# Optimization experiments

Hardware: AMD Instinct MI355X
Metric: run time of the kernel (lower is better)

Reference implementation:

```python
import jax, jax.numpy as jnp
import numpy as np


def _layer_norm(x, g, b, eps=1e-12):
    mu = jnp.mean(x, axis=-1, keepdims=True)
    var = jnp.mean(jnp.square(x - mu), axis=-1, keepdims=True)
    return (x - mu) * jax.lax.rsqrt(var + eps) * g + b


def setup_inputs() -> dict:
    B, S, H = 16, 512, 1024
    key = jax.random.key(0)
    ks = jax.random.split(key, 8)
    p = lambda k, sh: 0.02 * jax.random.normal(k, sh, jnp.float32)
    return {
        "sequence_output": jax.random.normal(ks[0], (B, S, H), jnp.float32),
        "p_mask": jax.random.randint(ks[1], (B, S), 0, 2).astype(jnp.float32),
        "w_start": p(ks[2], (H, 1)),
        "b_start": jnp.zeros((1,), jnp.float32),
        "w_end0": p(ks[3], (2 * H, H)),
        "b_end0": jnp.zeros((H,), jnp.float32),
        "ln_g": jnp.ones((H,), jnp.float32),
        "ln_b": jnp.zeros((H,), jnp.float32),
        "w_end1": p(ks[4], (H, 1)),
        "b_end1": jnp.zeros((1,), jnp.float32),
        "w_ans0": p(ks[5], (2 * H, H)),
        "b_ans0": jnp.zeros((H,), jnp.float32),
        "w_ans1": p(ks[6], (H, 1)),
        "start_n_top": 5,
        "end_n_top": 5,
    }


def reference(sequence_output, p_mask, w_start, b_start, w_end0, b_end0,
              ln_g, ln_b, w_end1, b_end1, w_ans0, b_ans0, w_ans1,
              start_n_top, end_n_top):
    # Inference (beam-search) branch of ALBertQALayer. Layout kept as [B,S,H]
    # (original transposes to [S,B,H]; math is identical).
    B, S, H = sequence_output.shape
    NEG = jnp.float32(1e30)

    # ---- start logits ----
    start_logits = (sequence_output @ w_start).squeeze(-1) + b_start          # [B,S]
    start_masked = start_logits * (1.0 - p_mask) - NEG * p_mask
    start_log_probs = jax.nn.log_softmax(start_masked, axis=-1)
    start_top_log_probs, start_top_index = jax.lax.top_k(start_log_probs, start_n_top)  # [B,K1]

    # ---- end logits conditioned on top-k starts ----
    start_features = jnp.take_along_axis(
        sequence_output, start_top_index[:, :, None], axis=1)                 # [B,K1,H]
    end_input = jnp.concatenate([
        jnp.broadcast_to(sequence_output[:, :, None, :], (B, S, start_n_top, H)),
        jnp.broadcast_to(start_features[:, None, :, :], (B, S, start_n_top, H)),
    ], axis=-1)                                                               # [B,S,K1,2H]
    end_h = jnp.tanh(jnp.einsum('bskd,dh->bskh', end_input, w_end0) + b_end0)
    end_h = _layer_norm(end_h, ln_g, ln_b)
    end_logits = jnp.einsum('bskh,ho->bsko', end_h, w_end1).squeeze(-1) + b_end1  # [B,S,K1]
    end_logits = jnp.transpose(end_logits, (0, 2, 1))                         # [B,K1,S]
    end_masked = end_logits * (1.0 - p_mask[:, None, :]) - NEG * p_mask[:, None, :]
    end_log_probs = jax.nn.log_softmax(end_masked, axis=-1)
    end_top_log_probs, end_top_index = jax.lax.top_k(end_log_probs, end_n_top)  # [B,K1,K2]
    end_top_log_probs = end_top_log_probs.reshape(B, start_n_top * end_n_top)
    end_top_index = end_top_index.reshape(B, start_n_top * end_n_top)

    # ---- answer-class (is-impossible) logits ----
    cls_feature = sequence_output[:, 0, :]                                    # one_hot(0) gather
    start_p = jax.nn.softmax(start_masked, axis=-1)
    start_feature = jnp.einsum('bs,bsh->bh', start_p, sequence_output)
    ans = jnp.tanh(jnp.concatenate([start_feature, cls_feature], axis=-1) @ w_ans0 + b_ans0)
    cls_logits = (ans @ w_ans1).squeeze(-1)                                   # [B]

    return (start_top_log_probs, start_top_index,
            end_top_log_probs, end_top_index, cls_logits)
```

## Files before the change

kernel.cpp:

```cpp
#include <hip/hip_runtime.h>
#include <math.h>

#define BB 16
#define SS 512
#define HH 1024
#define KT 5
#define NEGV 1e30f

typedef __attribute__((ext_vector_type(8))) short short8_t;
typedef __attribute__((ext_vector_type(4))) float f32x4;

__device__ __forceinline__ float wave_sum(float v) {
    for (int off = 32; off; off >>= 1) v += __shfl_down(v, off);
    return v;
}

__device__ __forceinline__ unsigned short bf16rn(float x) {
    unsigned u = __float_as_uint(x);
    return (unsigned short)((u + 0x7fffu + ((u >> 16) & 1u)) >> 16);
}

__device__ __forceinline__ void split2(float x, unsigned short& h, unsigned short& l) {
    h = bf16rn(x);
    float hf = __uint_as_float(((unsigned)h) << 16);
    l = bf16rn(x - hf);
}

__device__ __forceinline__ float tanh_fast(float x) {
    float e = __expf(2.0f * x);
    return 1.0f - 2.0f * __builtin_amdgcn_rcpf(e + 1.0f);
}

__device__ __forceinline__ void gld16(const short* g, char* l) {
    __builtin_amdgcn_global_load_lds((const __attribute__((address_space(1))) void*)g,
                                     (__attribute__((address_space(3))) void*)l, 16, 0, 0);
}

template <bool WRITE_P>
__device__ void softmax_topk_vals(float x0, float x1, float* __restrict__ p_out,
                                  float* __restrict__ val_out, float* __restrict__ idxf_out,
                                  int* __restrict__ idxi_out) {
    const int t = threadIdx.x;
    __shared__ float scr[4];
    __shared__ float sv[4];
    __shared__ int si[4];
    __shared__ int wi_s;

    float m = fmaxf(x0, x1);
    for (int off = 32; off; off >>= 1) m = fmaxf(m, __shfl_down(m, off));
    if ((t & 63) == 0) scr[t >> 6] = m;
    __syncthreads();
    m = fmaxf(fmaxf(scr[0], scr[1]), fmaxf(scr[2], scr[3]));
    __syncthreads();

    float e0 = expf(x0 - m), e1 = expf(x1 - m);
    float ssum = wave_sum(e0 + e1);
    if ((t & 63) == 0) scr[t >> 6] = ssum;
    __syncthreads();
    ssum = scr[0] + scr[1] + scr[2] + scr[3];
    __syncthreads();

    if (WRITE_P) {
        p_out[t] = e0 / ssum;
        p_out[t + 256] = e1 / ssum;
    }
    const float lse = m + logf(ssum);

    float v0 = x0, v1 = x1;
    for (int k = 0; k < KT; ++k) {
        float bv;
        int bi;
        if (v0 >= v1) { bv = v0; bi = t; } else { bv = v1; bi = t + 256; }
        for (int off = 32; off; off >>= 1) {
            float ov = __shfl_down(bv, off);
            int oi = __shfl_down(bi, off);
            if (ov > bv || (ov == bv && oi < bi)) { bv = ov; bi = oi; }
        }
        if ((t & 63) == 0) { sv[t >> 6] = bv; si[t >> 6] = bi; }
        __syncthreads();
        if (t == 0) {
            float fv = sv[0];
            int fi = si[0];
            for (int w = 1; w < 4; ++w)
                if (sv[w] > fv || (sv[w] == fv && si[w] < fi)) { fv = sv[w]; fi = si[w]; }
            wi_s = fi;
            val_out[k] = fv - lse;
            idxf_out[k] = (float)fi;
            if (idxi_out) idxi_out[k] = fi;
        }
        __syncthreads();
        const int wi = wi_s;
        if (wi == t) v0 = -INFINITY;
        else if (wi == t + 256) v1 = -INFINITY;
        __syncthreads();
    }
}

__global__ void k_mega(const float* __restrict__ seq, const float* __restrict__ w_end0,
                       const float* __restrict__ pm, const float* __restrict__ w_start,
                       const float* __restrict__ b_start, const float* __restrict__ ln_g,
                       const float* __restrict__ ln_b, const float* __restrict__ w_end1,
                       short* __restrict__ wpk_hi, short* __restrict__ wpk_lo,
                       short* __restrict__ apk_hi, short* __restrict__ apk_lo,
                       float* __restrict__ sm, float* __restrict__ scal) {
    const int bid = blockIdx.x;
    const int t = threadIdx.x;
    __shared__ float scr8[8];

    if (bid < 4096) {
        const size_t g = (size_t)bid * 256 + t;
        const int l = g & 63;
        const int mtl = (g >> 6) & 7;
        const int ks = (g >> 9) & 31;
        const int bm = g >> 14;
        const int row = bm * 128 + mtl * 16 + (l & 15);
        const int k0 = ks * 32 + (l >> 4) * 8;
        const float4 v0 = *(const float4*)(seq + (size_t)row * HH + k0);
        const float4 v1 = *(const float4*)(seq + (size_t)row * HH + k0 + 4);
        float xs[8] = {v0.x, v0.y, v0.z, v0.w, v1.x, v1.y, v1.z, v1.w};
        unsigned short h[8], lo[8];
#pragma unroll
        for (int j = 0; j < 8; ++j) split2(xs[j], h[j], lo[j]);
        short8_t hv, lv;
#pragma unroll
        for (int j = 0; j < 8; ++j) { hv[j] = (short)h[j]; lv[j] = (short)lo[j]; }
        *(short8_t*)(apk_hi + g * 8) = hv;
        *(short8_t*)(apk_lo + g * 8) = lv;
    } else if (bid < 4608) {
        const int bid2 = bid - 4096;
        const int nt = bid2 & 63;
        const int yy = bid2 >> 6;
        const int n_idx = t & 15;
        const int g = (t >> 4) & 3;
        const int kq = t >> 6;
        const int kblk = yy * 4 + kq;
        const int k0 = kblk * 32 + g * 8;
        unsigned short hs[8], ls[8];
#pragma unroll
        for (int j = 0; j < 8; ++j) {
            float v = w_end0[(size_t)(k0 + j) * HH + nt * 16 + n_idx];
            split2(v, hs[j], ls[j]);
        }
        const size_t fi = (((size_t)nt * 32 + kblk) * 64 + (g * 16 + n_idx)) * 8;
        short8_t hv, lv;
#pragma unroll
        for (int j = 0; j < 8; ++j) { hv[j] = (short)hs[j]; lv[j] = (short)ls[j]; }
        *(short8_t*)(wpk_hi + fi) = hv;
        *(short8_t*)(wpk_lo + fi) = lv;
    } else if (bid < 6656) {
        const int l = t & 63;
        const int row = (bid - 4608) * 4 + (t >> 6);
        const float4* rp = (const float4*)(seq + (size_t)row * HH);
        const float4* wp = (const float4*)w_start;
        float d = 0.f;
#pragma unroll
        for (int q = 0; q < 4; ++q) {
            float4 a = rp[q * 64 + l];
            float4 w = wp[q * 64 + l];
            d += a.x * w.x + a.y * w.y + a.z * w.z + a.w * w.w;
        }
        d = wave_sum(d);
        if (l == 0) {
            float m = pm[row];
            sm[row] = (d + b_start[0]) * (1.f - m) - NEGV * m;
        }
    } else {
        float4 g = ((const float4*)ln_g)[t];
        float4 w = ((const float4*)w_end1)[t];
        float4 b = ((const float4*)ln_b)[t];
        float gw = g.x * w.x + g.y * w.y + g.z * w.z + g.w * w.w;
        float bw = b.x * w.x + b.y * w.y + b.z * w.z + b.w * w.w;
        gw = wave_sum(gw);
        bw = wave_sum(bw);
        if ((t & 63) == 0) { scr8[t >> 6] = gw; scr8[4 + (t >> 6)] = bw; }
        __syncthreads();
        if (t == 0) {
            scal[0] = scr8[0] + scr8[1] + scr8[2] + scr8[3];
            scal[1] = scr8[4] + scr8[5] + scr8[6] + scr8[7];
        }
    }
}

__global__ void k_softmax_start(const float* __restrict__ sm, float* __restrict__ sp,
                                float* __restrict__ dout, int* __restrict__ idx) {
    const int b = blockIdx.x;
    const int t = threadIdx.x;
    const float* x = sm + (size_t)b * SS;
    softmax_topk_vals<true>(x[t], x[t + 256], sp + (size_t)b * SS,
                            dout + b * KT, dout + 80 + b * KT, idx + b * KT);
}

__global__ void k_mid(const float* __restrict__ seq, const int* __restrict__ idx,
                      const float* __restrict__ w_end0, float* __restrict__ Cpart,
                      const float* __restrict__ sp, float* __restrict__ partial) {
    __shared__ float shA[80 * 132];
    __shared__ float shW[16 * 132];
    __shared__ int growL[80];
    const int bid = blockIdx.x;
    const int t = threadIdx.x;

    if (bid < 512) {
        const int c = bid & 63;
        const int kc = bid >> 6;
        if (t < 80) growL[t] = (t / KT) * SS + idx[t];
        __syncthreads();
        for (int i = 0; i < 40; ++i) {
            const int e = i * 256 + t;
            const int r = e >> 7, d = e & 127;
            shA[r * 132 + d] = seq[(size_t)growL[r] * HH + kc * 128 + d];
        }
#pragma unroll
        for (int p = 0; p < 8; ++p) {
            const int e = p * 256 + t;
            const int d = e >> 4, j = e & 15;
            shW[j * 132 + d] = w_end0[(size_t)(HH + kc * 128 + d) * HH + c * 16 + j];
        }
        __syncthreads();
        const int j = t & 15, rg = t >> 4;
        const float4* A4 = (const float4*)shA;
        const float4* W4 = (const float4*)shW;
        float acc[5] = {0.f, 0.f, 0.f, 0.f, 0.f};
        for (int d4 = 0; d4 < 32; ++d4) {
            float4 wv = W4[j * 33 + d4];
#pragma unroll
            for (int i = 0; i < 5; ++i) {
                float4 av = A4[(rg + 16 * i) * 33 + d4];
                acc[i] += av.x * wv.x + av.y * wv.y + av.z * wv.z + av.w * wv.w;
            }
        }
#pragma unroll
        for (int i = 0; i < 5; ++i)
            Cpart[((size_t)kc * 80 + rg + 16 * i) * HH + c * 16 + j] = acc[i];
    } else {
        const int bid2 = bid - 512;
        const int chunk = bid2 & 31;
        const int b = bid2 >> 5;
        if (t < 16) shA[t] = sp[b * SS + chunk * 16 + t];
        __syncthreads();
        float4 acc = make_float4(0.f, 0.f, 0.f, 0.f);
        const float4* base = (const float4*)(seq + ((size_t)b * SS + chunk * 16) * HH);
        for (int s = 0; s < 16; ++s) {
            float4 v = base[(size_t)s * 256 + t];
            float ps = shA[s];
            acc.x = fmaf(ps, v.x, acc.x);
            acc.y = fmaf(ps, v.y, acc.y);
            acc.z = fmaf(ps, v.z, acc.z);
            acc.w = fmaf(ps, v.w, acc.w);
        }
        ((float4*)partial)[(size_t)(b * 32 + chunk) * 256 + t] = acc;
    }
}

__global__ void k_red(const float* __restrict__ Cpart, const float* __restrict__ b_end0,
                      float* __restrict__ Cb, const float* __restrict__ seq,
                      const float* __restrict__ partial, float* __restrict__ feat) {
    const int bid = blockIdx.x;
    const int t = threadIdx.x;
    if (bid < 80) {
        const int bk = bid;
#pragma unroll
        for (int q = 0; q < 4; ++q) {
            const int h = q * 256 + t;
            float s = b_end0[h];
#pragma unroll
            for (int kc = 0; kc < 8; ++kc) s += Cpart[((size_t)kc * 80 + bk) * HH + h];
            Cb[(size_t)bk * HH + h] = s;
        }
    } else {
        const int b = bid - 80;
        for (int q = 0; q < 4; ++q) {
            const int h = q * 256 + t;
            float s = 0.f;
            for (int c = 0; c < 32; ++c) s += partial[(size_t)(b * 32 + c) * HH + h];
            feat[(size_t)b * 2048 + h] = s;
            feat[(size_t)b * 2048 + HH + h] = seq[(size_t)b * SS * HH + h];
        }
    }
}

__global__ void k_ans(const float* __restrict__ feat, const float* __restrict__ w_ans0,
                      float* __restrict__ anspart) {
    __shared__ float A[16 * 132];
    __shared__ float W[16 * 132];
    const int c = blockIdx.x & 63;
    const int kc = blockIdx.x >> 6;
    const int t = threadIdx.x;
#pragma unroll
    for (int i = 0; i < 8; ++i) {
        const int e = i * 256 + t;
        const int b = e >> 7, d = e & 127;
        A[b * 132 + d] = feat[(size_t)b * 2048 + kc * 128 + d];
    }
#pragma unroll
    for (int p = 0; p < 8; ++p) {
        const int e = p * 256 + t;
        const int d = e >> 4, j = e & 15;
        W[j * 132 + d] = w_ans0[(size_t)(kc * 128 + d) * HH + c * 16 + j];
    }
    __syncthreads();
    const int j = t & 15, b = t >> 4;
    const float4* A4 = (const float4*)A;
    const float4* W4 = (const float4*)W;
    float acc = 0.f;
    for (int d4 = 0; d4 < 32; ++d4) {
        float4 wv = W4[j * 33 + d4];
        float4 av = A4[b * 33 + d4];
        acc += av.x * wv.x + av.y * wv.y + av.z * wv.z + av.w * wv.w;
    }
    anspart[((size_t)kc * 16 + b) * HH + c * 16 + j] = acc;
}

__global__ __launch_bounds__(256, 2)
void k_gemm(const short* __restrict__ apk_hi, const short* __restrict__ apk_lo,
            const short* __restrict__ wpk_hi, const short* __restrict__ wpk_lo,
            const float* __restrict__ Cb, const float* __restrict__ ln_g,
            const float* __restrict__ w_end1, float* __restrict__ part) {
    extern __shared__ char smem[];
    const int t = threadIdx.x;
    const int l = t & 63, w = t >> 6;
    const int wr = w >> 1, wc = w & 1;
    const int wg = blockIdx.x;
    const int xcd = wg & 7;
    const int local = wg >> 3;
    const int bm = xcd * 8 + (local >> 3);
    const int bn = local & 7;
    const int row0 = bm * 128;
    const int b = row0 >> 9;

    f32x4 acc[4][4];
#pragma unroll
    for (int m = 0; m < 4; ++m)
#pragma unroll
        for (int n = 0; n < 4; ++n) acc[m][n] = (f32x4){0.f, 0.f, 0.f, 0.f};

#define STAGE(buf, ks)                                                                   \
    {                                                                                    \
        const size_t abase = (size_t)(bm * 32 + (ks)) * 8 * 512;                         \
        const size_t wbase = ((size_t)(bn * 8) * 32 + (ks)) * 512;                       \
        char* lb = smem + (buf) * 32768;                                                 \
        _Pragma("unroll") for (int q = 0; q < 2; ++q) {                                  \
            const int fr = w + q * 4;                                                    \
            gld16(apk_hi + abase + fr * 512 + l * 8, lb + fr * 1024);                    \
            gld16(apk_lo + abase + fr * 512 + l * 8, lb + 8192 + fr * 1024);             \
            gld16(wpk_hi + wbase + (size_t)fr * 32 * 512 + l * 8, lb + 16384 + fr * 1024); \
            gld16(wpk_lo + wbase + (size_t)fr * 32 * 512 + l * 8, lb + 24576 + fr * 1024); \
        }                                                                                \
    }

    STAGE(0, 0);
    __syncthreads();

    for (int ks = 0; ks < 32; ++ks) {
        const int buf = ks & 1;
        if (ks < 31) STAGE(buf ^ 1, ks + 1);
        {
            const char* base_ = smem + buf * 32768;
            short8_t ah[4], al[4], wh[4], wl[4];
#pragma unroll
            for (int m = 0; m < 4; ++m) {
                const int mtl = wr * 4 + m;
                ah[m] = *(const short8_t*)(base_ + (mtl << 10) + (l << 4));
                al[m] = *(const short8_t*)(base_ + 8192 + (mtl << 10) + (l << 4));
            }
#pragma unroll
            for (int n = 0; n < 4; ++n) {
                const int ntl = wc * 4 + n;
                wh[n] = *(const short8_t*)(base_ + 16384 + (ntl << 10) + (l << 4));
                wl[n] = *(const short8_t*)(base_ + 24576 + (ntl << 10) + (l << 4));
            }
#pragma unroll
            for (int n = 0; n < 4; ++n)
#pragma unroll
                for (int m = 0; m < 4; ++m) {
                    acc[m][n] = __builtin_amdgcn_mfma_f32_16x16x32_bf16(ah[m], wh[n], acc[m][n], 0, 0, 0);
                    acc[m][n] = __builtin_amdgcn_mfma_f32_16x16x32_bf16(al[m], wh[n], acc[m][n], 0, 0, 0);
                    acc[m][n] = __builtin_amdgcn_mfma_f32_16x16x32_bf16(ah[m], wl[n], acc[m][n], 0, 0, 0);
                }
        }
        __syncthreads();
    }
#undef STAGE

    float cbv[KT][4], gwv[4];
#pragma unroll
    for (int n = 0; n < 4; ++n) {
        const int col = bn * 128 + wc * 64 + n * 16 + (l & 15);
        gwv[n] = ln_g[col] * w_end1[col];
#pragma unroll
        for (int k = 0; k < KT; ++k) cbv[k][n] = Cb[(size_t)(b * KT + k) * HH + col];
    }
    float* scr = (float*)smem;

    for (int k = 0; k < KT; ++k) {
        float S[4][4], Q[4][4], G[4][4];
#pragma unroll
        for (int m = 0; m < 4; ++m)
#pragma unroll
            for (int r = 0; r < 4; ++r) { S[m][r] = 0.f; Q[m][r] = 0.f; G[m][r] = 0.f; }
#pragma unroll
        for (int n = 0; n < 4; ++n) {
            const float cb = cbv[k][n];
            const float gwn = gwv[n];
#pragma unroll
            for (int m = 0; m < 4; ++m)
#pragma unroll
                for (int r = 0; r < 4; ++r) {
                    float v = tanh_fast(acc[m][n][r] + cb);
                    S[m][r] += v;
                    Q[m][r] += v * v;
                    G[m][r] += v * gwn;
                }
        }
        for (int msk = 1; msk < 16; msk <<= 1) {
#pragma unroll
            for (int m = 0; m < 4; ++m)
#pragma unroll
                for (int r = 0; r < 4; ++r) {
                    S[m][r] += __shfl_xor(S[m][r], msk);
                    Q[m][r] += __shfl_xor(Q[m][r], msk);
                    G[m][r] += __shfl_xor(G[m][r], msk);
                }
        }
        if ((l & 15) == 0) {
            const int gg = l >> 4;
#pragma unroll
            for (int m = 0; m < 4; ++m)
#pragma unroll
                for (int r = 0; r < 4; ++r) {
                    const int row = wr * 64 + m * 16 + gg * 4 + r;
                    float* sp_ = scr + ((wc * 128 + row) * KT + k) * 3;
                    sp_[0] = S[m][r];
                    sp_[1] = Q[m][r];
                    sp_[2] = G[m][r];
                }
        }
    }
    __syncthreads();

#pragma unroll
    for (int i = 0; i < 3; ++i) {
        const int idx = i * 256 + t;
        if (idx < 128 * KT) {
            const int row = idx / KT, k = idx % KT;
            const float* a_ = scr + ((0 * 128 + row) * KT + k) * 3;
            const float* b_ = scr + ((1 * 128 + row) * KT + k) * 3;
            float4 o;
            o.x = a_[0] + b_[0];
            o.y = a_[1] + b_[1];
            o.z = a_[2] + b_[2];
            o.w = 0.f;
            *(float4*)(part + (((size_t)bn * (BB * SS) + row0 + row) * KT + k) * 4) = o;
        }
    }
}

__global__ void k_final(const float* __restrict__ part, const float* __restrict__ p_mask,
                        const float* __restrict__ scal, const float* __restrict__ b_end1,
                        const float* __restrict__ anspart, const float* __restrict__ b_ans0,
                        const float* __restrict__ w_ans1, float* __restrict__ out) {
    const int bid = blockIdx.x;
    const int t = threadIdx.x;
    __shared__ float rscr[4];

    if (bid < 80) {
        const int b = bid / KT, k = bid % KT;
        const float GW1 = scal[0], BW1 = scal[1], be1 = b_end1[0];
        float x01[2];
#pragma unroll
        for (int h = 0; h < 2; ++h) {
            const int s = h * 256 + t;
            const int row = b * SS + s;
            float S = 0.f, Q = 0.f, G = 0.f;
#pragma unroll
            for (int bn = 0; bn < 8; ++bn) {
                float4 v = *(const float4*)(part + (((size_t)bn * (BB * SS) + row) * KT + k) * 4);
                S += v.x;
                Q += v.y;
                G += v.z;
            }
            const float mu = S * (1.f / HH);
            const float var = Q * (1.f / HH) - mu * mu;
            const float rs = rsqrtf(var + 1e-12f);
            const float logit = rs * (G - mu * GW1) + BW1 + be1;
            const float pm = p_mask[row];
            x01[h] = logit * (1.f - pm) - NEGV * pm;
        }
        softmax_topk_vals<false>(x01[0], x01[1], nullptr,
                                 out + 160 + b * 25 + k * KT, out + 560 + b * 25 + k * KT, nullptr);
    } else {
        const int b = bid - 80;
        float dsum = 0.f;
#pragma unroll
        for (int q = 0; q < 4; ++q) {
            const int h = q * 256 + t;
            float s = b_ans0[h];
#pragma unroll
            for (int kc = 0; kc < 16; ++kc) s += anspart[((size_t)kc * 16 + b) * HH + h];
            dsum += tanhf(s) * w_ans1[h];
        }
        dsum = wave_sum(dsum);
        if ((t & 63) == 0) rscr[t >> 6] = dsum;
        __syncthreads();
        if (t == 0) out[960 + b] = rscr[0] + rscr[1] + rscr[2] + rscr[3];
    }
}

extern "C" void kernel_launch(void* const* d_in, const int* in_sizes, int n_in,
                              void* d_out, int out_size, void* d_ws, size_t ws_size,
                              hipStream_t stream) {
    const float* seq     = (const float*)d_in[0];
    const float* p_mask  = (const float*)d_in[1];
    const float* w_start = (const float*)d_in[2];
    const float* b_start = (const float*)d_in[3];
    const float* w_end0  = (const float*)d_in[4];
    const float* b_end0  = (const float*)d_in[5];
    const float* ln_g    = (const float*)d_in[6];
    const float* ln_b    = (const float*)d_in[7];
    const float* w_end1  = (const float*)d_in[8];
    const float* b_end1  = (const float*)d_in[9];
    const float* w_ans0  = (const float*)d_in[10];
    const float* b_ans0  = (const float*)d_in[11];
    const float* w_ans1  = (const float*)d_in[12];
    float* out = (float*)d_out;

    float* sm      = (float*)d_ws;
    float* sp      = sm + BB * SS;
    float* partial = sp + BB * SS;
    float* feat    = partial + BB * 32 * HH;
    float* Cb      = feat + BB * 2048;
    float* Cpart   = Cb + 80 * HH;
    float* anspart = Cpart + 8 * 80 * HH;
    float* scal    = anspart + 16 * BB * HH;
    int*   idx     = (int*)(scal + 16);
    float* part    = (float*)(((uintptr_t)(idx + 80) + 255) & ~(uintptr_t)255);
    short* wpk_hi  = (short*)(part + 8 * BB * SS * KT * 4);
    short* wpk_lo  = wpk_hi + (1 << 20);
    short* apk_hi  = wpk_lo + (1 << 20);
    short* apk_lo  = apk_hi + (1 << 23);

    hipLaunchKernelGGL(k_mega, dim3(6657), dim3(256), 0, stream,
                       seq, w_end0, p_mask, w_start, b_start, ln_g, ln_b, w_end1,
                       wpk_hi, wpk_lo, apk_hi, apk_lo, sm, scal);
    hipLaunchKernelGGL(k_softmax_start, dim3(BB), dim3(256), 0, stream, sm, sp, out, idx);
    hipLaunchKernelGGL(k_mid, dim3(1024), dim3(256), 0, stream,
                       seq, idx, w_end0, Cpart, sp, partial);
    hipLaunchKernelGGL(k_red, dim3(96), dim3(256), 0, stream,
                       Cpart, b_end0, Cb, seq, partial, feat);
    hipLaunchKernelGGL(k_ans, dim3(1024), dim3(256), 0, stream, feat, w_ans0, anspart);
    hipLaunchKernelGGL(k_gemm, dim3(512), dim3(256), 65536, stream,
                       apk_hi, apk_lo, wpk_hi, wpk_lo, Cb, ln_g, w_end1, part);
    hipLaunchKernelGGL(k_final, dim3(96), dim3(256), 0, stream,
                       part, p_mask, scal, b_end1, anspart, b_ans0, w_ans1, out);
}
```

Before: 129.7 us.

## Load GEMM weight fragments directly to registers, halve LDS, raise occupancy

In k_gemm the split-bf16 weight tiles (hi/lo) are now loaded straight from global memory into registers, with the hi part prefetched one k-step ahead, instead of being staged through LDS. Only the activation tiles stay double-buffered in shared memory, which halves dynamic LDS from 64KB to 32KB, and launch bounds are raised to 3 blocks per CU. The MFMA section is also wrapped in s_setprio. The aim is to cut LDS traffic and footprint so more blocks fit per CU, at the cost of more register pressure and direct global loads that each wave issues separately for its own weight columns.

```diff
diff --git a/kernel.cpp b/kernel.cpp
--- a/kernel.cpp
+++ b/kernel.cpp
@@ -310,7 +310,7 @@
     anspart[((size_t)kc * 16 + b) * HH + c * 16 + j] = acc;
 }
 
-__global__ __launch_bounds__(256, 2)
+__global__ __launch_bounds__(256, 3)
 void k_gemm(const short* __restrict__ apk_hi, const short* __restrict__ apk_lo,
             const short* __restrict__ wpk_hi, const short* __restrict__ wpk_lo,
             const float* __restrict__ Cb, const float* __restrict__ ln_g,
@@ -333,49 +333,61 @@
 #pragma unroll
         for (int n = 0; n < 4; ++n) acc[m][n] = (f32x4){0.f, 0.f, 0.f, 0.f};
 
-#define STAGE(buf, ks)                                                                   \
-    {                                                                                    \
-        const size_t abase = (size_t)(bm * 32 + (ks)) * 8 * 512;                         \
-        const size_t wbase = ((size_t)(bn * 8) * 32 + (ks)) * 512;                       \
-        char* lb = smem + (buf) * 32768;                                                 \
-        _Pragma("unroll") for (int q = 0; q < 2; ++q) {                                  \
-            const int fr = w + q * 4;                                                    \
-            gld16(apk_hi + abase + fr * 512 + l * 8, lb + fr * 1024);                    \
-            gld16(apk_lo + abase + fr * 512 + l * 8, lb + 8192 + fr * 1024);             \
-            gld16(wpk_hi + wbase + (size_t)fr * 32 * 512 + l * 8, lb + 16384 + fr * 1024); \
-            gld16(wpk_lo + wbase + (size_t)fr * 32 * 512 + l * 8, lb + 24576 + fr * 1024); \
-        }                                                                                \
-    }
+    const short8_t* WH = (const short8_t*)wpk_hi;
+    const short8_t* WL = (const short8_t*)wpk_lo;
+    const size_t wb = ((size_t)(bn * 8 + wc * 4)) * 2048 + l;
+
+#define STAGE(buf, ks)                                                     \
+    {                                                                      \
+        const size_t abase = (size_t)(bm * 32 + (ks)) * 4096;              \
+        char* lb = smem + (buf) * 16384;                                   \
+        gld16(apk_hi + abase + (2 * w) * 512 + l * 8, lb + (2 * w) * 1024);        \
+        gld16(apk_hi + abase + (2 * w + 1) * 512 + l * 8, lb + (2 * w + 1) * 1024); \
+        gld16(apk_lo + abase + (2 * w) * 512 + l * 8, lb + 8192 + (2 * w) * 1024);  \
+        gld16(apk_lo + abase + (2 * w + 1) * 512 + l * 8, lb + 8192 + (2 * w + 1) * 1024); \
+    }
+
+    short8_t wCh[4], wNh[4], wl_[4];
 
     STAGE(0, 0);
+#pragma unroll
+    for (int n = 0; n < 4; ++n) wCh[n] = WH[wb + n * 2048];
     __syncthreads();
 
     for (int ks = 0; ks < 32; ++ks) {
         const int buf = ks & 1;
-        if (ks < 31) STAGE(buf ^ 1, ks + 1);
-        {
-            const char* base_ = smem + buf * 32768;
-            short8_t ah[4], al[4], wh[4], wl[4];
+        if (ks < 31) {
+            STAGE(buf ^ 1, ks + 1);
+#pragma unroll
+            for (int n = 0; n < 4; ++n) wNh[n] = WH[wb + n * 2048 + (ks + 1) * 64];
+        }
+#pragma unroll
+        for (int n = 0; n < 4; ++n) wl_[n] = WL[wb + n * 2048 + ks * 64];
+        const char* base_ = smem + buf * 16384;
+        short8_t ah[4], al[4];
+#pragma unroll
+        for (int m = 0; m < 4; ++m) {
+            const int mtl = wr * 4 + m;
+            ah[m] = *(const short8_t*)(base_ + (mtl << 10) + (l << 4));
+            al[m] = *(const short8_t*)(base_ + 8192 + (mtl << 10) + (l << 4));
+        }
+        __builtin_amdgcn_s_setprio(1);
+#pragma unroll
+        for (int n = 0; n < 4; ++n)
 #pragma unroll
             for (int m = 0; m < 4; ++m) {
-                const int mtl = wr * 4 + m;
-                ah[m] = *(const short8_t*)(base_ + (mtl << 10) + (l << 4));
-                al[m] = *(const short8_t*)(base_ + 8192 + (mtl << 10) + (l << 4));
+                acc[m][n] = __builtin_amdgcn_mfma_f32_16x16x32_bf16(ah[m], wCh[n], acc[m][n], 0, 0, 0);
+                acc[m][n] = __builtin_amdgcn_mfma_f32_16x16x32_bf16(al[m], wCh[n], acc[m][n], 0, 0, 0);
             }
 #pragma unroll
-            for (int n = 0; n < 4; ++n) {
-                const int ntl = wc * 4 + n;
-                wh[n] = *(const short8_t*)(base_ + 16384 + (ntl << 10) + (l << 4));
-                wl[n] = *(const short8_t*)(base_ + 24576 + (ntl << 10) + (l << 4));
-            }
-#pragma unroll
-            for (int n = 0; n < 4; ++n)
-#pragma unroll
-                for (int m = 0; m < 4; ++m) {
-                    acc[m][n] = __builtin_amdgcn_mfma_f32_16x16x32_bf16(ah[m], wh[n], acc[m][n], 0, 0, 0);
-                    acc[m][n] = __builtin_amdgcn_mfma_f32_16x16x32_bf16(al[m], wh[n], acc[m][n], 0, 0, 0);
-                    acc[m][n] = __builtin_amdgcn_mfma_f32_16x16x32_bf16(ah[m], wl[n], acc[m][n], 0, 0, 0);
-                }
+        for (int n = 0; n < 4; ++n)
+#pragma unroll
+            for (int m = 0; m < 4; ++m)
+                acc[m][n] = __builtin_amdgcn_mfma_f32_16x16x32_bf16(ah[m], wl_[n], acc[m][n], 0, 0, 0);
+        __builtin_amdgcn_s_setprio(0);
+        if (ks < 31) {
+#pragma unroll
+            for (int n = 0; n < 4; ++n) wCh[n] = wNh[n];
         }
         __syncthreads();
     }
@@ -547,7 +559,7 @@
     hipLaunchKernelGGL(k_red, dim3(96), dim3(256), 0, stream,
                        Cpart, b_end0, Cb, seq, partial, feat);
     hipLaunchKernelGGL(k_ans, dim3(1024), dim3(256), 0, stream, feat, w_ans0, anspart);
-    hipLaunchKernelGGL(k_gemm, dim3(512), dim3(256), 65536, stream,
+    hipLaunchKernelGGL(k_gemm, dim3(512), dim3(256), 32768, stream,
                        apk_hi, apk_lo, wpk_hi, wpk_lo, Cb, ln_g, w_end1, part);
     hipLaunchKernelGGL(k_final, dim3(96), dim3(256), 0, stream,
                        part, p_mask, scal, b_end1, anspart, b_ans0, w_ans1, out);
```

Result: no change. 131.3 us (+1.2%).

## Fuse activation bf16 hi/lo split into GEMM, loading fp32 seq directly to LDS

Applied to the files above, without the earlier changes.

Drops the pre-pass in the mega kernel that split the 32 MB fp32 sequence into packed bf16 hi/lo buffers. The GEMM now streams fp32 rows straight into LDS with an XOR swizzle and does the split in registers before the MFMAs. This removes a full write and re-read of the packed activations, at the cost of extra ALU work and LDS reads inside the GEMM inner loop. It also raises wave priority around the MFMA block.

```diff
diff --git a/kernel.cpp b/kernel.cpp
--- a/kernel.cpp
+++ b/kernel.cpp
@@ -31,7 +31,7 @@
     return 1.0f - 2.0f * __builtin_amdgcn_rcpf(e + 1.0f);
 }
 
-__device__ __forceinline__ void gld16(const short* g, char* l) {
+__device__ __forceinline__ void gld16(const void* g, char* l) {
     __builtin_amdgcn_global_load_lds((const __attribute__((address_space(1))) void*)g,
                                      (__attribute__((address_space(3))) void*)l, 16, 0, 0);
 }
@@ -101,35 +101,14 @@
                        const float* __restrict__ b_start, const float* __restrict__ ln_g,
                        const float* __restrict__ ln_b, const float* __restrict__ w_end1,
                        short* __restrict__ wpk_hi, short* __restrict__ wpk_lo,
-                       short* __restrict__ apk_hi, short* __restrict__ apk_lo,
                        float* __restrict__ sm, float* __restrict__ scal) {
     const int bid = blockIdx.x;
     const int t = threadIdx.x;
     __shared__ float scr8[8];
 
-    if (bid < 4096) {
-        const size_t g = (size_t)bid * 256 + t;
-        const int l = g & 63;
-        const int mtl = (g >> 6) & 7;
-        const int ks = (g >> 9) & 31;
-        const int bm = g >> 14;
-        const int row = bm * 128 + mtl * 16 + (l & 15);
-        const int k0 = ks * 32 + (l >> 4) * 8;
-        const float4 v0 = *(const float4*)(seq + (size_t)row * HH + k0);
-        const float4 v1 = *(const float4*)(seq + (size_t)row * HH + k0 + 4);
-        float xs[8] = {v0.x, v0.y, v0.z, v0.w, v1.x, v1.y, v1.z, v1.w};
-        unsigned short h[8], lo[8];
-#pragma unroll
-        for (int j = 0; j < 8; ++j) split2(xs[j], h[j], lo[j]);
-        short8_t hv, lv;
-#pragma unroll
-        for (int j = 0; j < 8; ++j) { hv[j] = (short)h[j]; lv[j] = (short)lo[j]; }
-        *(short8_t*)(apk_hi + g * 8) = hv;
-        *(short8_t*)(apk_lo + g * 8) = lv;
-    } else if (bid < 4608) {
-        const int bid2 = bid - 4096;
-        const int nt = bid2 & 63;
-        const int yy = bid2 >> 6;
+    if (bid < 512) {
+        const int nt = bid & 63;
+        const int yy = bid >> 6;
         const int n_idx = t & 15;
         const int g = (t >> 4) & 3;
         const int kq = t >> 6;
@@ -147,9 +126,9 @@
         for (int j = 0; j < 8; ++j) { hv[j] = (short)hs[j]; lv[j] = (short)ls[j]; }
         *(short8_t*)(wpk_hi + fi) = hv;
         *(short8_t*)(wpk_lo + fi) = lv;
-    } else if (bid < 6656) {
+    } else if (bid < 2560) {
         const int l = t & 63;
-        const int row = (bid - 4608) * 4 + (t >> 6);
+        const int row = (bid - 512) * 4 + (t >> 6);
         const float4* rp = (const float4*)(seq + (size_t)row * HH);
         const float4* wp = (const float4*)w_start;
         float d = 0.f;
@@ -311,10 +290,10 @@
 }
 
 __global__ __launch_bounds__(256, 2)
-void k_gemm(const short* __restrict__ apk_hi, const short* __restrict__ apk_lo,
-            const short* __restrict__ wpk_hi, const short* __restrict__ wpk_lo,
-            const float* __restrict__ Cb, const float* __restrict__ ln_g,
-            const float* __restrict__ w_end1, float* __restrict__ part) {
+void k_gemm(const float* __restrict__ seq, const short* __restrict__ wpk_hi,
+            const short* __restrict__ wpk_lo, const float* __restrict__ Cb,
+            const float* __restrict__ ln_g, const float* __restrict__ w_end1,
+            float* __restrict__ part) {
     extern __shared__ char smem[];
     const int t = threadIdx.x;
     const int l = t & 63, w = t >> 6;
@@ -333,22 +312,42 @@
 #pragma unroll
         for (int n = 0; n < 4; ++n) acc[m][n] = (f32x4){0.f, 0.f, 0.f, 0.f};
 
-#define STAGE(buf, ks)                                                                   \
-    {                                                                                    \
-        const size_t abase = (size_t)(bm * 32 + (ks)) * 8 * 512;                         \
-        const size_t wbase = ((size_t)(bn * 8) * 32 + (ks)) * 512;                       \
-        char* lb = smem + (buf) * 32768;                                                 \
-        _Pragma("unroll") for (int q = 0; q < 2; ++q) {                                  \
-            const int fr = w + q * 4;                                                    \
-            gld16(apk_hi + abase + fr * 512 + l * 8, lb + fr * 1024);                    \
-            gld16(apk_lo + abase + fr * 512 + l * 8, lb + 8192 + fr * 1024);             \
-            gld16(wpk_hi + wbase + (size_t)fr * 32 * 512 + l * 8, lb + 16384 + fr * 1024); \
-            gld16(wpk_lo + wbase + (size_t)fr * 32 * 512 + l * 8, lb + 24576 + fr * 1024); \
-        }                                                                                \
+    const float* asrc[4];
+    int adst[4];
+#pragma unroll
+    for (int q = 0; q < 4; ++q) {
+        const int i = w * 256 + q * 64 + l;
+        const int row = i >> 3;
+        const int c = (i & 7) ^ (row & 7);
+        asrc[q] = seq + ((size_t)(row0 + row) << 10) + c * 4;
+        adst[q] = i * 16;
+    }
+    const short* wsrc_hi[2];
+    const short* wsrc_lo[2];
+    int wdst[2];
+#pragma unroll
+    for (int q = 0; q < 2; ++q) {
+        const int fr = w + q * 4;
+        wsrc_hi[q] = wpk_hi + ((size_t)(bn * 8 + fr) * 32) * 512 + l * 8;
+        wsrc_lo[q] = wpk_lo + ((size_t)(bn * 8 + fr) * 32) * 512 + l * 8;
+        wdst[q] = fr * 1024;
+    }
+
+#define STAGE(buf, ks)                                                     \
+    {                                                                      \
+        char* lb = smem + (buf) * 32768;                                   \
+        _Pragma("unroll") for (int q = 0; q < 4; ++q)                      \
+            gld16(asrc[q] + (ks) * 32, lb + adst[q]);                      \
+        _Pragma("unroll") for (int q = 0; q < 2; ++q) {                    \
+            gld16(wsrc_hi[q] + (ks) * 512, lb + 16384 + wdst[q]);          \
+            gld16(wsrc_lo[q] + (ks) * 512, lb + 24576 + wdst[q]);          \
+        }                                                                  \
     }
 
     STAGE(0, 0);
     __syncthreads();
+
+    const int c0 = (l >> 4) << 1;
 
     for (int ks = 0; ks < 32; ++ks) {
         const int buf = ks & 1;
@@ -358,9 +357,27 @@
             short8_t ah[4], al[4], wh[4], wl[4];
 #pragma unroll
             for (int m = 0; m < 4; ++m) {
-                const int mtl = wr * 4 + m;
-                ah[m] = *(const short8_t*)(base_ + (mtl << 10) + (l << 4));
-                al[m] = *(const short8_t*)(base_ + 8192 + (mtl << 10) + (l << 4));
+                const int rowm = (wr * 4 + m) * 16 + (l & 15);
+                const int rb = rowm * 128;
+                const int sw = (rowm & 7) << 4;
+                float4 a0 = *(const float4*)(base_ + rb + ((c0 << 4) ^ sw));
+                float4 a1 = *(const float4*)(base_ + rb + (((c0 + 1) << 4) ^ sw));
+                unsigned short h0, g0, h1, g1, h2, g2, h3, g3, h4, g4, h5, g5, h6, g6, h7, g7;
+                split2(a0.x, h0, g0);
+                split2(a0.y, h1, g1);
+                split2(a0.z, h2, g2);
+                split2(a0.w, h3, g3);
+                split2(a1.x, h4, g4);
+                split2(a1.y, h5, g5);
+                split2(a1.z, h6, g6);
+                split2(a1.w, h7, g7);
+                short8_t hv, lv;
+                hv[0] = (short)h0; hv[1] = (short)h1; hv[2] = (short)h2; hv[3] = (short)h3;
+                hv[4] = (short)h4; hv[5] = (short)h5; hv[6] = (short)h6; hv[7] = (short)h7;
+                lv[0] = (short)g0; lv[1] = (short)g1; lv[2] = (short)g2; lv[3] = (short)g3;
+                lv[4] = (short)g4; lv[5] = (short)g5; lv[6] = (short)g6; lv[7] = (short)g7;
+                ah[m] = hv;
+                al[m] = lv;
             }
 #pragma unroll
             for (int n = 0; n < 4; ++n) {
@@ -368,6 +385,7 @@
                 wh[n] = *(const short8_t*)(base_ + 16384 + (ntl << 10) + (l << 4));
                 wl[n] = *(const short8_t*)(base_ + 24576 + (ntl << 10) + (l << 4));
             }
+            __builtin_amdgcn_s_setprio(1);
 #pragma unroll
             for (int n = 0; n < 4; ++n)
 #pragma unroll
@@ -376,6 +394,7 @@
                     acc[m][n] = __builtin_amdgcn_mfma_f32_16x16x32_bf16(al[m], wh[n], acc[m][n], 0, 0, 0);
                     acc[m][n] = __builtin_amdgcn_mfma_f32_16x16x32_bf16(ah[m], wl[n], acc[m][n], 0, 0, 0);
                 }
+            __builtin_amdgcn_s_setprio(0);
         }
         __syncthreads();
     }
@@ -535,12 +554,10 @@
     float* part    = (float*)(((uintptr_t)(idx + 80) + 255) & ~(uintptr_t)255);
     short* wpk_hi  = (short*)(part + 8 * BB * SS * KT * 4);
     short* wpk_lo  = wpk_hi + (1 << 20);
-    short* apk_hi  = wpk_lo + (1 << 20);
-    short* apk_lo  = apk_hi + (1 << 23);
-
-    hipLaunchKernelGGL(k_mega, dim3(6657), dim3(256), 0, stream,
+
+    hipLaunchKernelGGL(k_mega, dim3(2561), dim3(256), 0, stream,
                        seq, w_end0, p_mask, w_start, b_start, ln_g, ln_b, w_end1,
-                       wpk_hi, wpk_lo, apk_hi, apk_lo, sm, scal);
+                       wpk_hi, wpk_lo, sm, scal);
     hipLaunchKernelGGL(k_softmax_start, dim3(BB), dim3(256), 0, stream, sm, sp, out, idx);
     hipLaunchKernelGGL(k_mid, dim3(1024), dim3(256), 0, stream,
                        seq, idx, w_end0, Cpart, sp, partial);
@@ -548,7 +565,7 @@
                        Cpart, b_end0, Cb, seq, partial, feat);
     hipLaunchKernelGGL(k_ans, dim3(1024), dim3(256), 0, stream, feat, w_ans0, anspart);
     hipLaunchKernelGGL(k_gemm, dim3(512), dim3(256), 65536, stream,
-                       apk_hi, apk_lo, wpk_hi, wpk_lo, Cb, ln_g, w_end1, part);
+                       seq, wpk_hi, wpk_lo, Cb, ln_g, w_end1, part);
     hipLaunchKernelGGL(k_final, dim3(96), dim3(256), 0, stream,
                        part, p_mask, scal, b_end1, anspart, b_ans0, w_ans1, out);
 }
```

Measured after the change: 135.9 us. 1.05x slower.
